# Performance work log

Measured on AMD Instinct MI355X. Metric: run time of the kernel, lower is better.

Reference implementation:

```python
import jax, jax.numpy as jnp
import numpy as np

L, H, D, DK, FF = 3, 8, 128, 16, 512  # layers, heads, embed, key/val dim, ffn hidden
B, N, F_IN, OUT = 32, 512, 16, 3
SCALE = 1.0 / np.sqrt(DK)


def setup_inputs() -> dict:
    key = jax.random.key(0)
    ks = jax.random.split(key, 16)
    x = jax.random.normal(ks[0], (B, N, F_IN), dtype=jnp.float32)
    m = jax.random.randint(ks[1], (B, N, N), 0, 2).astype(jnp.int32)
    # guarantee each query attends to at least itself (avoid all -inf rows)
    m = jnp.maximum(m, jnp.eye(N, dtype=jnp.int32)[None])
    def u(k, shape, fan):
        s = 1.0 / np.sqrt(fan)
        return jax.random.uniform(k, shape, jnp.float32, -s, s)
    return {
        "x": x, "mask": m,
        "We": u(ks[2], (F_IN, D), D),
        "Wq": u(ks[3], (L, H, D, DK), DK),
        "Wk": u(ks[4], (L, H, D, DK), DK),
        "Wv": u(ks[5], (L, H, D, DK), DK),
        "Wout": u(ks[6], (L, H, DK, D), D),
        "Wff1": u(ks[7], (L, D, FF), D),
        "bff1": u(ks[8], (L, FF), D),
        "Wff2": u(ks[9], (L, FF, D), FF),
        "bff2": u(ks[10], (L, D), FF),
        "Wp": u(ks[11], (D, D), D),
        "Wr": u(ks[12], (2 * D, OUT), 2 * D),
        "br": u(ks[13], (OUT,), 2 * D),
    }


def reference(x, mask, We, Wq, Wk, Wv, Wout, Wff1, bff1, Wff2, bff2, Wp, Wr, br):
    mb = mask.astype(bool)[None]  # [1,B,N,N] broadcast over heads
    h = jax.nn.relu(x @ We)  # initial embedding [B,N,D]
    for l in range(L):
        # multi-head attention with additive skip
        Q = jnp.einsum('bnd,hdk->hbnk', h, Wq[l])
        K = jnp.einsum('bnd,hdk->hbnk', h, Wk[l])
        V = jnp.einsum('bnd,hdk->hbnk', h, Wv[l])
        compat = SCALE * jnp.einsum('hbqk,hbnk->hbqn', Q, K)  # [H,B,N,N]
        compat = jnp.where(mb, compat, -jnp.inf)
        attn = jax.nn.softmax(compat, axis=-1)
        # note: torch's attn.clone()[...] = 0 is a no-op, so no re-zeroing
        heads = jnp.einsum('hbqn,hbnk->hbqk', attn, V)
        h = h + jnp.einsum('hbqk,hkd->bqd', heads, Wout[l])
        # feed-forward with additive skip
        h = h + jax.nn.relu(h @ Wff1[l] + bff1[l]) @ Wff2[l] + bff2[l] * 0 + (jax.nn.relu(h @ Wff1[l] + bff1[l]) @ Wff2[l] + bff2[l] - (jax.nn.relu(h @ Wff1[l] + bff1[l]) @ Wff2[l]))  # placeholder removed below
    return h


# clean faithful version (used)
def reference(x, mask, We, Wq, Wk, Wv, Wout, Wff1, bff1, Wff2, bff2, Wp, Wr, br):
    mb = mask.astype(bool)[None]  # [1,B,N,N]
    h = jax.nn.relu(x @ We)  # [B,N,D]
    for l in range(L):
        Q = jnp.einsum('bnd,hdk->hbnk', h, Wq[l])
        K = jnp.einsum('bnd,hdk->hbnk', h, Wk[l])
        V = jnp.einsum('bnd,hdk->hbnk', h, Wv[l])
        compat = SCALE * jnp.einsum('hbqk,hbnk->hbqn', Q, K)
        compat = jnp.where(mb, compat, -jnp.inf)
        attn = jax.nn.softmax(compat, axis=-1)
        heads = jnp.einsum('hbqn,hbnk->hbqk', attn, V)
        h = h + jnp.einsum('hbqk,hkd->bqd', heads, Wout[l])
        h = h + (jax.nn.relu(h @ Wff1[l] + bff1[l]) @ Wff2[l] + bff2[l])
    # readout (actor head: output_dim=3)
    h_pooled = (h.mean(axis=1)) @ Wp  # [B,D]
    f_pooled = jnp.broadcast_to(h_pooled[:, None, :], h.shape)  # [B,N,D]
    features = jax.nn.relu(jnp.concatenate([f_pooled, h], axis=-1))  # [B,N,2D]
    return features @ Wr + br  # [B,N,3]
```

## Files before the change

kernel.cpp:

```cpp
#include <hip/hip_runtime.h>
#include <cstdint>
#include <cstddef>

#define L_LAYERS 3
#define H_HEADS 8
#define D_EMB 128
#define DKV 16
#define FF_DIM 512
#define B_BATCH 32
#define N_SEQ 512
#define F_INP 16
#define OUT_DIM 3
#define M_ROWS (B_BATCH * N_SEQ)
#define QSCALE 0.3606737602222409f

typedef unsigned short ushort_t;
typedef unsigned int uint_t;
typedef __attribute__((ext_vector_type(8))) short short8;
typedef __attribute__((ext_vector_type(4))) float f32x4;
typedef __attribute__((ext_vector_type(16))) float f32x16;

__device__ inline ushort_t f2bf(float x) {
    union { float f; uint_t u; } v; v.f = x;
    uint_t r = v.u + 0x7fffu + ((v.u >> 16) & 1u);
    return (ushort_t)(r >> 16);
}

__device__ inline uint_t pack2bf_tr(float a, float b) {
    union { float f; uint_t u; } ua, ub;
    ua.f = a; ub.f = b;
#if __has_builtin(__builtin_amdgcn_perm)
    return __builtin_amdgcn_perm(ub.u, ua.u, 0x07060302u);
#else
    return (ua.u >> 16) | (ub.u & 0xffff0000u);
#endif
}

__device__ inline float exp2fast(float x) {
#if __has_builtin(__builtin_amdgcn_exp2f)
    return __builtin_amdgcn_exp2f(x);
#else
    float r; __asm__("v_exp_f32 %0, %1" : "=v"(r) : "v"(x)); return r;
#endif
}

__device__ inline void gload16(const void* g, void* l) {
    __builtin_amdgcn_global_load_lds(
        (const __attribute__((address_space(1))) unsigned int*)g,
        (__attribute__((address_space(3))) unsigned int*)l, 16, 0, 0);
}

#define PM_BLK 32768
#define RQ_BLK 576
#define TW_BLK 192
#define T1_BLK 768
#define T2_BLK 768
#define PB_BLK 16
#define EM_BLK 8192
__global__ __launch_bounds__(256) void preproc_kernel(
        const int* __restrict__ mask, unsigned long long* __restrict__ pm,
        const float* __restrict__ Wq, const float* __restrict__ Wk,
        const float* __restrict__ Wv, ushort_t* __restrict__ wqkvT,
        const float* __restrict__ Wout, ushort_t* __restrict__ woutT,
        const float* __restrict__ Wff1, ushort_t* __restrict__ wff1T,
        const float* __restrict__ Wff2, ushort_t* __restrict__ wff2T,
        float* __restrict__ pbsum,
        const float* __restrict__ x, const float* __restrict__ We,
        float* __restrict__ hf, ushort_t* __restrict__ hb) {
    int bx = blockIdx.x;
    const int tid = threadIdx.x;
    if (bx < PM_BLK) {
        int gid = bx * 256 + tid;
        int v = mask[gid];
        unsigned long long bal = __ballot(v != 0);
        if ((tid & 63) == 0) pm[gid >> 6] = bal;
        return;
    }
    bx -= PM_BLK;
    if (bx < RQ_BLK) {
        int idx = bx * 256 + tid;
        int d = idx & 127;
        int n = (idx >> 7) % 384;
        int l = idx / (384 * 128);
        int proj = n >> 7, hh = (n & 127) >> 4, kk = n & 15;
        const float* src = proj == 0 ? Wq : proj == 1 ? Wk : Wv;
        wqkvT[idx] = f2bf(src[((size_t)(l * 8 + hh) * 128 + d) * 16 + kk]);
        return;
    }
    bx -= RQ_BLK;
    if (bx < TW_BLK + T1_BLK + T2_BLK) {
        const float* src; ushort_t* dst; int R, C;
        if (bx < TW_BLK) { src = Wout; dst = woutT; R = 128; C = 128; }
        else if (bx < TW_BLK + T1_BLK) { src = Wff1; dst = wff1T; R = 128; C = 512; bx -= TW_BLK; }
        else { src = Wff2; dst = wff2T; R = 512; C = 128; bx -= TW_BLK + T1_BLK; }
        int idx = bx * 256 + tid;
        int b = idx / (R * C);
        int rem = idx - b * (R * C);
        int r = rem / C, c = rem - r * C;
        dst[(size_t)b * R * C + (size_t)c * R + r] = f2bf(src[idx]);
        return;
    }
    bx -= TW_BLK + T1_BLK + T2_BLK;
    if (bx < PB_BLK) {
        pbsum[bx * 256 + tid] = 0.f;
        return;
    }
    bx -= PB_BLK;
    {
        const int d = tid & 127;
        const int m = bx * 2 + (tid >> 7);
        const float* xr = x + (size_t)m * 16;
        float acc = 0.f;
#pragma unroll
        for (int k = 0; k < 16; k++) acc += xr[k] * We[k * 128 + d];
        acc = fmaxf(acc, 0.f);
        hf[(size_t)m * 128 + d] = acc;
        hb[(size_t)m * 128 + d] = f2bf(acc);
    }
}

__global__ __launch_bounds__(512, 4) void qkv_attn_kernel(
        const ushort_t* __restrict__ hb,
        const ushort_t* __restrict__ WqkvT,
        const uint_t* __restrict__ pm,
        ushort_t* __restrict__ Aout) {
    __shared__ __align__(16) ushort_t sm[35968];
    ushort_t* KF = sm;
    ushort_t* Vt = sm + 8192;
    ushort_t* Qs = sm + 16512;
    ushort_t* Ws = sm + 20608;
    ushort_t* Ps = sm + 16512;
    uint_t*   Ms = (uint_t*)(sm + 26752);

    const int tid = threadIdx.x;
    const int w = tid >> 6, L = tid & 63;
    const int lr = L & 15, lq = L >> 4;
    const int lane31 = L & 31, lhalf = L >> 5;
    const int bx = blockIdx.x;
    const int b = bx >> 4, h = (bx >> 1) & 7, half = bx & 1;

    for (int i = tid; i < 768; i += 512) {
        const int row = i >> 4, cg = i & 15;
        const int proj = row >> 4, kk = row & 15;
        gload16(WqkvT + (size_t)(proj * 128 + h * 16 + kk) * 128 + cg * 8, &Ws[i * 8]);
    }
    for (int i = tid; i < 2048; i += 512) {
        const int q = i >> 3, cw = (i & 7) * 2;
        const uint2 v = *(const uint2*)(pm + (size_t)(b * 512 + half * 256 + q) * 16 + cw);
        *(uint2*)&Ms[q * 18 + cw] = v;
    }
    __syncthreads();

    const ushort_t* Ab = hb + (size_t)b * 512 * 128;
    for (int mc = 0; mc < 4; mc++) {
        f32x4 acc[3];
#pragma unroll
        for (int j = 0; j < 3; j++) acc[j] = (f32x4){0.f, 0.f, 0.f, 0.f};
#pragma unroll
        for (int k0 = 0; k0 < 128; k0 += 32) {
            short8 af = *(const short8*)(Ab + (size_t)(mc * 128 + w * 16 + lr) * 128 + k0 + lq * 8);
#pragma unroll
            for (int j = 0; j < 3; j++) {
                short8 bf = *(const short8*)&Ws[(j * 16 + lr) * 128 + k0 + lq * 8];
                acc[j] = __builtin_amdgcn_mfma_f32_16x16x32_bf16(af, bf, acc[j], 0, 0, 0);
            }
        }
        const int rbase = mc * 128 + w * 16 + lq * 4;
#pragma unroll
        for (int r = 0; r < 4; r++) {
            const int key = rbase + r;
            KF[(key >> 5) * 512 + ((lr >> 3) * 32 + (key & 31)) * 8 + (lr & 7)] = f2bf(acc[1][r]);
            Vt[lr * 520 + key] = f2bf(acc[2][r]);
        }
        if ((mc >> 1) == half) {
            const int qb = (mc & 1) * 128 + w * 16 + lq * 4;
#pragma unroll
            for (int r = 0; r < 4; r++)
                Qs[(qb + r) * 16 + lr] = f2bf(acc[0][r] * QSCALE);
        }
    }
    __syncthreads();

    const int q0g = half * 256 + w * 32;
    const short8 qf = *(const short8*)&Qs[(w * 32 + lane31) * 16 + lhalf * 8];
    const int msrow = (w * 32 + lane31) * 18;
    __syncthreads();

    const f32x16 zero16 = (f32x16)(0.f);
    short8 vone;
#pragma unroll
    for (int i = 0; i < 8; i++) vone[i] = (short)0x3F80;

    f32x4 oacc0 = (f32x4){0.f, 0.f, 0.f, 0.f};
    f32x4 oacc1 = (f32x4){0.f, 0.f, 0.f, 0.f};
    f32x4 lacc0 = (f32x4){0.f, 0.f, 0.f, 0.f};
    f32x4 lacc1 = (f32x4){0.f, 0.f, 0.f, 0.f};
#pragma unroll
    for (int t = 0; t < 16; t++) {
        short8 kf = *(const short8*)&KF[t * 512 + L * 8];
        f32x16 s = __builtin_amdgcn_mfma_f32_32x32x16_bf16(kf, qf, zero16, 0, 0, 0);
        const uint_t word = Ms[msrow + t];
#pragma unroll
        for (int r = 0; r < 16; r++) {
            const int keyl = (r & 3) + 8 * (r >> 2) + 4 * lhalf;
            const float e = exp2fast(s[r]);
            s[r] = (word & (1u << keyl)) ? e : 0.f;
        }
#pragma unroll
        for (int g = 0; g < 4; g++) {
            const uint_t lo = pack2bf_tr(s[g * 4 + 0], s[g * 4 + 1]);
            const uint_t hi = pack2bf_tr(s[g * 4 + 2], s[g * 4 + 3]);
            *(uint2*)&Ps[w * 1152 + lane31 * 36 + g * 8 + 4 * lhalf] = make_uint2(lo, hi);
        }
        short8 vb = *(const short8*)&Vt[lr * 520 + t * 32 + lq * 8];
        short8 pa0 = *(const short8*)&Ps[w * 1152 + lr * 36 + lq * 8];
        short8 pa1 = *(const short8*)&Ps[w * 1152 + (16 + lr) * 36 + lq * 8];
        oacc0 = __builtin_amdgcn_mfma_f32_16x16x32_bf16(pa0, vb, oacc0, 0, 0, 0);
        oacc1 = __builtin_amdgcn_mfma_f32_16x16x32_bf16(pa1, vb, oacc1, 0, 0, 0);
        lacc0 = __builtin_amdgcn_mfma_f32_16x16x32_bf16(pa0, vone, lacc0, 0, 0, 0);
        lacc1 = __builtin_amdgcn_mfma_f32_16x16x32_bf16(pa1, vone, lacc1, 0, 0, 0);
    }

#pragma unroll
    for (int qa = 0; qa < 2; qa++) {
        const f32x4 oa = qa ? oacc1 : oacc0;
        const f32x4 la = qa ? lacc1 : lacc0;
#pragma unroll
        for (int rr = 0; rr < 4; rr++) {
            const int qloc = qa * 16 + lq * 4 + rr;
            Aout[(size_t)(b * 512 + q0g + qloc) * 128 + h * 16 + lr] = f2bf(oa[rr] / la[rr]);
        }
    }
}

__global__ __launch_bounds__(256, 2) void tail_kernel(
        const ushort_t* __restrict__ A,
        const ushort_t* __restrict__ WoT,
        const ushort_t* __restrict__ W1T,
        const ushort_t* __restrict__ W2T,
        const float* __restrict__ b1,
        const float* __restrict__ b2,
        float* __restrict__ hf, ushort_t* __restrict__ hb,
        float* __restrict__ pbsum, int accum) {
    __shared__ __align__(16) ushort_t sm[39424];
    ushort_t* AsA = sm;
    ushort_t* AsB = sm + 1024;
    ushort_t* BsA = sm + 2048;
    ushort_t* BsB = sm + 10240;
    ushort_t* C1b = sm + 18432;
    ushort_t* T   = sm + 22784;

    const int tid = threadIdx.x;
    const int w = tid >> 6, l = tid & 63;
    const int lr = l & 15, lq = l >> 4;
    const int srow = (l >> 2);
    const int scol = (l & 3) * 8;
    const int m0 = blockIdx.x * 32;

    f32x4 c1a[2][2];
#pragma unroll
    for (int i = 0; i < 2; i++)
#pragma unroll
        for (int j = 0; j < 2; j++) c1a[i][j] = (f32x4){0.f, 0.f, 0.f, 0.f};
    if (w < 2)
        gload16(A + (size_t)(m0 + w * 16 + srow) * 128 + scol, &AsA[(w * 16 + srow) * 32 + scol]);
#pragma unroll
    for (int it = 0; it < 2; it++)
        gload16(WoT + (size_t)(it * 64 + w * 16 + srow) * 128 + scol, &BsA[(it * 64 + w * 16 + srow) * 32 + scol]);
#pragma unroll
    for (int k0 = 0; k0 < 128; k0 += 32) {
        ushort_t* Ac = (k0 & 32) ? AsB : AsA;
        ushort_t* Bc = (k0 & 32) ? BsB : BsA;
        ushort_t* An = (k0 & 32) ? AsA : AsB;
        ushort_t* Bn = (k0 & 32) ? BsA : BsB;
        __syncthreads();
        if (k0 + 32 < 128) {
            if (w < 2)
                gload16(A + (size_t)(m0 + w * 16 + srow) * 128 + k0 + 32 + scol,
                        &An[(w * 16 + srow) * 32 + scol]);
#pragma unroll
            for (int it = 0; it < 2; it++)
                gload16(WoT + (size_t)(it * 64 + w * 16 + srow) * 128 + k0 + 32 + scol,
                        &Bn[(it * 64 + w * 16 + srow) * 32 + scol]);
        }
        short8 af[2], bfr[2];
#pragma unroll
        for (int i = 0; i < 2; i++) af[i] = *(const short8*)&Ac[(i * 16 + lr) * 32 + lq * 8];
#pragma unroll
        for (int j = 0; j < 2; j++) bfr[j] = *(const short8*)&Bc[(w * 32 + j * 16 + lr) * 32 + lq * 8];
#pragma unroll
        for (int i = 0; i < 2; i++)
#pragma unroll
            for (int j = 0; j < 2; j++)
                c1a[i][j] = __builtin_amdgcn_mfma_f32_16x16x32_bf16(af[i], bfr[j], c1a[i][j], 0, 0, 0);
    }
    float c1[2][2][4];
#pragma unroll
    for (int i = 0; i < 2; i++)
#pragma unroll
        for (int r = 0; r < 4; r++) {
            const int row = i * 16 + lq * 4 + r;
#pragma unroll
            for (int j = 0; j < 2; j++) {
                const int n = w * 32 + j * 16 + lr;
                const float v = c1a[i][j][r] + hf[(size_t)(m0 + row) * 128 + n];
                c1[i][j][r] = v;
                C1b[row * 136 + n] = f2bf(v);
            }
        }

#pragma unroll
    for (int it = 0; it < 4; it++)
        gload16(W1T + (size_t)(it * 64 + w * 16 + srow) * 128 + scol, &BsA[(it * 64 + w * 16 + srow) * 32 + scol]);
#pragma unroll
    for (int nc = 0; nc < 2; nc++) {
        f32x4 ta[2][4];
#pragma unroll
        for (int i = 0; i < 2; i++)
#pragma unroll
            for (int j = 0; j < 4; j++) ta[i][j] = (f32x4){0.f, 0.f, 0.f, 0.f};
#pragma unroll
        for (int k0i = 0; k0i < 4; k0i++) {
            const int c = nc * 4 + k0i;
            ushort_t* Bc = (c & 1) ? BsB : BsA;
            ushort_t* Bn = (c & 1) ? BsA : BsB;
            __syncthreads();
            if (c + 1 < 8) {
                const int nc2 = (c + 1) >> 2, k02 = ((c + 1) & 3) * 32;
#pragma unroll
                for (int it = 0; it < 4; it++)
                    gload16(W1T + (size_t)(nc2 * 256 + it * 64 + w * 16 + srow) * 128 + k02 + scol,
                            &Bn[(it * 64 + w * 16 + srow) * 32 + scol]);
            }
            short8 af[2], bfr[4];
#pragma unroll
            for (int i = 0; i < 2; i++)
                af[i] = *(const short8*)&C1b[(i * 16 + lr) * 136 + k0i * 32 + lq * 8];
#pragma unroll
            for (int j = 0; j < 4; j++)
                bfr[j] = *(const short8*)&Bc[(w * 64 + j * 16 + lr) * 32 + lq * 8];
#pragma unroll
            for (int i = 0; i < 2; i++)
#pragma unroll
                for (int j = 0; j < 4; j++)
                    ta[i][j] = __builtin_amdgcn_mfma_f32_16x16x32_bf16(af[i], bfr[j], ta[i][j], 0, 0, 0);
        }
#pragma unroll
        for (int j = 0; j < 4; j++) {
            const int n = nc * 256 + w * 64 + j * 16 + lr;
            const float bv = b1[n];
#pragma unroll
            for (int i = 0; i < 2; i++)
#pragma unroll
                for (int r = 0; r < 4; r++) {
                    const int row = i * 16 + lq * 4 + r;
                    T[row * 520 + n] = f2bf(fmaxf(ta[i][j][r] + bv, 0.f));
                }
        }
    }

#pragma unroll
    for (int it = 0; it < 2; it++)
        gload16(W2T + (size_t)(it * 64 + w * 16 + srow) * 512 + scol, &BsA[(it * 64 + w * 16 + srow) * 32 + scol]);
    f32x4 oa[2][2];
#pragma unroll
    for (int i = 0; i < 2; i++)
#pragma unroll
        for (int j = 0; j < 2; j++) oa[i][j] = (f32x4){0.f, 0.f, 0.f, 0.f};
#pragma unroll
    for (int k0 = 0; k0 < 512; k0 += 32) {
        ushort_t* Bc = ((k0 >> 5) & 1) ? BsB : BsA;
        ushort_t* Bn = ((k0 >> 5) & 1) ? BsA : BsB;
        __syncthreads();
        if (k0 + 32 < 512) {
#pragma unroll
            for (int it = 0; it < 2; it++)
                gload16(W2T + (size_t)(it * 64 + w * 16 + srow) * 512 + k0 + 32 + scol,
                        &Bn[(it * 64 + w * 16 + srow) * 32 + scol]);
        }
        short8 af[2], bfr[2];
#pragma unroll
        for (int i = 0; i < 2; i++)
            af[i] = *(const short8*)&T[(i * 16 + lr) * 520 + k0 + lq * 8];
#pragma unroll
        for (int j = 0; j < 2; j++)
            bfr[j] = *(const short8*)&Bc[(w * 32 + j * 16 + lr) * 32 + lq * 8];
#pragma unroll
        for (int i = 0; i < 2; i++)
#pragma unroll
            for (int j = 0; j < 2; j++)
                oa[i][j] = __builtin_amdgcn_mfma_f32_16x16x32_bf16(af[i], bfr[j], oa[i][j], 0, 0, 0);
    }
#pragma unroll
    for (int j = 0; j < 2; j++) {
        const int n = w * 32 + j * 16 + lr;
        const float bv = b2[n];
        float psum = 0.f;
#pragma unroll
        for (int i = 0; i < 2; i++)
#pragma unroll
            for (int r = 0; r < 4; r++) {
                const int row = i * 16 + lq * 4 + r;
                const float v = oa[i][j][r] + bv + c1[i][j][r];
                psum += v;
                hf[(size_t)(m0 + row) * 128 + n] = v;
                hb[(size_t)(m0 + row) * 128 + n] = f2bf(v);
            }
        if (accum) {
            psum += __shfl_xor(psum, 16);
            psum += __shfl_xor(psum, 32);
            if (lq == 0) atomicAdd(&pbsum[(m0 >> 9) * 128 + n], psum);
        }
    }
}

__global__ __launch_bounds__(256) void readout_kernel(const float* __restrict__ h,
                                                      const float* __restrict__ pbsum,
                                                      const float* __restrict__ Wp,
                                                      const float* __restrict__ Wr,
                                                      const float* __restrict__ br,
                                                      float* __restrict__ out) {
    const int u = blockIdx.x;
    const int b = u >> 4;
    const int m0 = u * 32;
    const int t = threadIdx.x;
    __shared__ float pooled[128];
    __shared__ float rp[128];
    __shared__ float pb3[3];
    if (t < 128) pooled[t] = pbsum[b * 128 + t] * (1.0f / 512.0f);
    __syncthreads();
    if (t < 128) {
        float a = 0.f;
        for (int dd = 0; dd < 128; dd++) a += pooled[dd] * Wp[dd * 128 + t];
        rp[t] = fmaxf(a, 0.f);
    }
    __syncthreads();
    if (t < OUT_DIM) {
        float a = br[t];
        for (int j = 0; j < 128; j++) a += rp[j] * Wr[j * 3 + t];
        pb3[t] = a;
    }
    __syncthreads();
    const int j = t & 7;
    const int row = m0 + (t >> 3);
    const float* hr = h + (size_t)row * 128 + j * 16;
    float a0 = 0.f, a1 = 0.f, a2o = 0.f;
#pragma unroll
    for (int dd = 0; dd < 16; dd++) {
        const float v = fmaxf(hr[dd], 0.f);
        const float* wr = Wr + (size_t)(128 + j * 16 + dd) * 3;
        a0 += v * wr[0]; a1 += v * wr[1]; a2o += v * wr[2];
    }
#pragma unroll
    for (int off = 4; off; off >>= 1) {
        a0 += __shfl_down(a0, off, 8);
        a1 += __shfl_down(a1, off, 8);
        a2o += __shfl_down(a2o, off, 8);
    }
    if (j == 0) {
        out[(size_t)row * 3 + 0] = a0 + pb3[0];
        out[(size_t)row * 3 + 1] = a1 + pb3[1];
        out[(size_t)row * 3 + 2] = a2o + pb3[2];
    }
}

extern "C" void kernel_launch(void* const* d_in, const int* in_sizes, int n_in,
                              void* d_out, int out_size, void* d_ws, size_t ws_size,
                              hipStream_t stream) {
    const float* x    = (const float*)d_in[0];
    const int*   mask = (const int*)d_in[1];
    const float* We   = (const float*)d_in[2];
    const float* Wq   = (const float*)d_in[3];
    const float* Wk   = (const float*)d_in[4];
    const float* Wv   = (const float*)d_in[5];
    const float* Wout = (const float*)d_in[6];
    const float* Wff1 = (const float*)d_in[7];
    const float* bff1 = (const float*)d_in[8];
    const float* Wff2 = (const float*)d_in[9];
    const float* bff2 = (const float*)d_in[10];
    const float* Wp   = (const float*)d_in[11];
    const float* Wr   = (const float*)d_in[12];
    const float* br   = (const float*)d_in[13];
    float* out = (float*)d_out;

    char* ws = (char*)d_ws;
    unsigned long long* pm64 = (unsigned long long*)(ws + 0);
    const uint_t* pm32       = (const uint_t*)(ws + 0);
    ushort_t* wqkvT = (ushort_t*)(ws + 1048576);
    ushort_t* woutT = (ushort_t*)(ws + 1343488);
    ushort_t* wff1T = (ushort_t*)(ws + 1441792);
    ushort_t* wff2T = (ushort_t*)(ws + 1835008);
    float*    pbsum = (float*)(ws + 2228224);
    float*    hbuf  = (float*)(ws + 4194304);
    ushort_t* hb16  = (ushort_t*)(ws + 12582912);
    ushort_t* a16   = (ushort_t*)(ws + 41943040);

    preproc_kernel<<<PM_BLK + RQ_BLK + TW_BLK + T1_BLK + T2_BLK + PB_BLK + EM_BLK, 256, 0, stream>>>(
        mask, pm64, Wq, Wk, Wv, wqkvT, Wout, woutT, Wff1, wff1T, Wff2, wff2T,
        pbsum, x, We, hbuf, hb16);

    for (int l = 0; l < L_LAYERS; l++) {
        qkv_attn_kernel<<<512, 512, 0, stream>>>(
            hb16, wqkvT + (size_t)l * 384 * 128, pm32, a16);
        tail_kernel<<<M_ROWS / 32, 256, 0, stream>>>(
            a16, woutT + (size_t)l * 128 * 128, wff1T + (size_t)l * 512 * 128,
            wff2T + (size_t)l * 128 * 512, bff1 + l * 512, bff2 + l * 128,
            hbuf, hb16, pbsum, (l == L_LAYERS - 1) ? 1 : 0);
    }

    readout_kernel<<<512, 256, 0, stream>>>(hbuf, pbsum, Wp, Wr, br, out);
}
```

Before: 276.2 us.

## Stream tail weights from global, split FFN hidden into halves, double-buffer attention P

The tail kernel stops staging A, Wout, Wff1 and Wff2 through LDS with double-buffered global_load_lds and instead reads MFMA operands straight from global memory through cache. It also splits the FFN hidden dimension into two halves so the intermediate tile and LDS footprint shrink, using XOR-swizzled layouts to avoid bank conflicts. In the attention kernel, P is ping-ponged between two LDS buffers, and the PV MFMAs are wrapped in s_setprio. Attention occupancy drops from 4 to 2 blocks per CU, and direct global weight loads risk higher latency in exchange for fewer barriers.

```diff
diff --git a/kernel.cpp b/kernel.cpp
--- a/kernel.cpp
+++ b/kernel.cpp
@@ -48,6 +48,13 @@
     __builtin_amdgcn_global_load_lds(
         (const __attribute__((address_space(1))) unsigned int*)g,
         (__attribute__((address_space(3))) unsigned int*)l, 16, 0, 0);
+}
+
+__device__ inline int swz128(int row, int col) {
+    return row * 128 + ((((col >> 3) ^ (row & 7)) << 3) | (col & 7));
+}
+__device__ inline int swz256(int row, int col) {
+    return row * 256 + ((((col >> 3) ^ (row & 7)) << 3) | (col & 7));
 }
 
 #define PM_BLK 32768
@@ -119,18 +126,19 @@
     }
 }
 
-__global__ __launch_bounds__(512, 4) void qkv_attn_kernel(
+__global__ __launch_bounds__(512, 2) void qkv_attn_kernel(
         const ushort_t* __restrict__ hb,
         const ushort_t* __restrict__ WqkvT,
         const uint_t* __restrict__ pm,
         ushort_t* __restrict__ Aout) {
-    __shared__ __align__(16) ushort_t sm[35968];
-    ushort_t* KF = sm;
-    ushort_t* Vt = sm + 8192;
-    ushort_t* Qs = sm + 16512;
-    ushort_t* Ws = sm + 20608;
-    ushort_t* Ps = sm + 16512;
-    uint_t*   Ms = (uint_t*)(sm + 26752);
+    __shared__ __align__(16) ushort_t sm[44160];
+    ushort_t* KF  = sm;
+    ushort_t* Vt  = sm + 8192;
+    ushort_t* Qs  = sm + 16512;
+    ushort_t* Ws  = sm + 20608;
+    ushort_t* PsA = sm + 16512;
+    ushort_t* PsB = sm + 25728;
+    uint_t*   Ms  = (uint_t*)(sm + 34944);
 
     const int tid = threadIdx.x;
     const int w = tid >> 6, L = tid & 63;
@@ -195,31 +203,40 @@
     f32x4 oacc1 = (f32x4){0.f, 0.f, 0.f, 0.f};
     f32x4 lacc0 = (f32x4){0.f, 0.f, 0.f, 0.f};
     f32x4 lacc1 = (f32x4){0.f, 0.f, 0.f, 0.f};
-#pragma unroll
-    for (int t = 0; t < 16; t++) {
-        short8 kf = *(const short8*)&KF[t * 512 + L * 8];
-        f32x16 s = __builtin_amdgcn_mfma_f32_32x32x16_bf16(kf, qf, zero16, 0, 0, 0);
-        const uint_t word = Ms[msrow + t];
-#pragma unroll
-        for (int r = 0; r < 16; r++) {
-            const int keyl = (r & 3) + 8 * (r >> 2) + 4 * lhalf;
-            const float e = exp2fast(s[r]);
-            s[r] = (word & (1u << keyl)) ? e : 0.f;
-        }
-#pragma unroll
-        for (int g = 0; g < 4; g++) {
-            const uint_t lo = pack2bf_tr(s[g * 4 + 0], s[g * 4 + 1]);
-            const uint_t hi = pack2bf_tr(s[g * 4 + 2], s[g * 4 + 3]);
-            *(uint2*)&Ps[w * 1152 + lane31 * 36 + g * 8 + 4 * lhalf] = make_uint2(lo, hi);
-        }
-        short8 vb = *(const short8*)&Vt[lr * 520 + t * 32 + lq * 8];
-        short8 pa0 = *(const short8*)&Ps[w * 1152 + lr * 36 + lq * 8];
-        short8 pa1 = *(const short8*)&Ps[w * 1152 + (16 + lr) * 36 + lq * 8];
-        oacc0 = __builtin_amdgcn_mfma_f32_16x16x32_bf16(pa0, vb, oacc0, 0, 0, 0);
-        oacc1 = __builtin_amdgcn_mfma_f32_16x16x32_bf16(pa1, vb, oacc1, 0, 0, 0);
-        lacc0 = __builtin_amdgcn_mfma_f32_16x16x32_bf16(pa0, vone, lacc0, 0, 0, 0);
-        lacc1 = __builtin_amdgcn_mfma_f32_16x16x32_bf16(pa1, vone, lacc1, 0, 0, 0);
-    }
+
+#define ATTN_STEP(T_IDX, PS) do {                                                   \
+    short8 kf = *(const short8*)&KF[(T_IDX) * 512 + L * 8];                         \
+    f32x16 s = __builtin_amdgcn_mfma_f32_32x32x16_bf16(kf, qf, zero16, 0, 0, 0);    \
+    const uint_t word = Ms[msrow + (T_IDX)];                                        \
+    _Pragma("unroll")                                                               \
+    for (int r = 0; r < 16; r++) {                                                  \
+        const int keyl = (r & 3) + 8 * (r >> 2) + 4 * lhalf;                        \
+        const float e = exp2fast(s[r]);                                             \
+        s[r] = (word & (1u << keyl)) ? e : 0.f;                                     \
+    }                                                                               \
+    _Pragma("unroll")                                                               \
+    for (int g = 0; g < 4; g++) {                                                   \
+        const uint_t lo = pack2bf_tr(s[g * 4 + 0], s[g * 4 + 1]);                   \
+        const uint_t hi = pack2bf_tr(s[g * 4 + 2], s[g * 4 + 3]);                   \
+        *(uint2*)&(PS)[w * 1152 + lane31 * 36 + g * 8 + 4 * lhalf] = make_uint2(lo, hi); \
+    }                                                                               \
+    short8 vb = *(const short8*)&Vt[lr * 520 + (T_IDX) * 32 + lq * 8];              \
+    short8 pa0 = *(const short8*)&(PS)[w * 1152 + lr * 36 + lq * 8];                \
+    short8 pa1 = *(const short8*)&(PS)[w * 1152 + (16 + lr) * 36 + lq * 8];         \
+    __builtin_amdgcn_s_setprio(1);                                                  \
+    oacc0 = __builtin_amdgcn_mfma_f32_16x16x32_bf16(pa0, vb, oacc0, 0, 0, 0);       \
+    oacc1 = __builtin_amdgcn_mfma_f32_16x16x32_bf16(pa1, vb, oacc1, 0, 0, 0);       \
+    lacc0 = __builtin_amdgcn_mfma_f32_16x16x32_bf16(pa0, vone, lacc0, 0, 0, 0);     \
+    lacc1 = __builtin_amdgcn_mfma_f32_16x16x32_bf16(pa1, vone, lacc1, 0, 0, 0);     \
+    __builtin_amdgcn_s_setprio(0);                                                  \
+} while (0)
+
+#pragma unroll
+    for (int tp = 0; tp < 8; tp++) {
+        ATTN_STEP(2 * tp, PsA);
+        ATTN_STEP(2 * tp + 1, PsB);
+    }
+#undef ATTN_STEP
 
 #pragma unroll
     for (int qa = 0; qa < 2; qa++) {
@@ -242,19 +259,13 @@
         const float* __restrict__ b2,
         float* __restrict__ hf, ushort_t* __restrict__ hb,
         float* __restrict__ pbsum, int accum) {
-    __shared__ __align__(16) ushort_t sm[39424];
-    ushort_t* AsA = sm;
-    ushort_t* AsB = sm + 1024;
-    ushort_t* BsA = sm + 2048;
-    ushort_t* BsB = sm + 10240;
-    ushort_t* C1b = sm + 18432;
-    ushort_t* T   = sm + 22784;
+    __shared__ __align__(16) ushort_t sm[12288];
+    ushort_t* C1b = sm;
+    ushort_t* Tt  = sm + 4096;
 
     const int tid = threadIdx.x;
     const int w = tid >> 6, l = tid & 63;
     const int lr = l & 15, lq = l >> 4;
-    const int srow = (l >> 2);
-    const int scol = (l & 3) * 8;
     const int m0 = blockIdx.x * 32;
 
     f32x4 c1a[2][2];
@@ -262,32 +273,15 @@
     for (int i = 0; i < 2; i++)
 #pragma unroll
         for (int j = 0; j < 2; j++) c1a[i][j] = (f32x4){0.f, 0.f, 0.f, 0.f};
-    if (w < 2)
-        gload16(A + (size_t)(m0 + w * 16 + srow) * 128 + scol, &AsA[(w * 16 + srow) * 32 + scol]);
-#pragma unroll
-    for (int it = 0; it < 2; it++)
-        gload16(WoT + (size_t)(it * 64 + w * 16 + srow) * 128 + scol, &BsA[(it * 64 + w * 16 + srow) * 32 + scol]);
 #pragma unroll
     for (int k0 = 0; k0 < 128; k0 += 32) {
-        ushort_t* Ac = (k0 & 32) ? AsB : AsA;
-        ushort_t* Bc = (k0 & 32) ? BsB : BsA;
-        ushort_t* An = (k0 & 32) ? AsA : AsB;
-        ushort_t* Bn = (k0 & 32) ? BsA : BsB;
-        __syncthreads();
-        if (k0 + 32 < 128) {
-            if (w < 2)
-                gload16(A + (size_t)(m0 + w * 16 + srow) * 128 + k0 + 32 + scol,
-                        &An[(w * 16 + srow) * 32 + scol]);
-#pragma unroll
-            for (int it = 0; it < 2; it++)
-                gload16(WoT + (size_t)(it * 64 + w * 16 + srow) * 128 + k0 + 32 + scol,
-                        &Bn[(it * 64 + w * 16 + srow) * 32 + scol]);
-        }
         short8 af[2], bfr[2];
 #pragma unroll
-        for (int i = 0; i < 2; i++) af[i] = *(const short8*)&Ac[(i * 16 + lr) * 32 + lq * 8];
-#pragma unroll
-        for (int j = 0; j < 2; j++) bfr[j] = *(const short8*)&Bc[(w * 32 + j * 16 + lr) * 32 + lq * 8];
+        for (int i = 0; i < 2; i++)
+            af[i] = *(const short8*)(A + (size_t)(m0 + i * 16 + lr) * 128 + k0 + lq * 8);
+#pragma unroll
+        for (int j = 0; j < 2; j++)
+            bfr[j] = *(const short8*)(WoT + (size_t)(w * 32 + j * 16 + lr) * 128 + k0 + lq * 8);
 #pragma unroll
         for (int i = 0; i < 2; i++)
 #pragma unroll
@@ -305,92 +299,70 @@
                 const int n = w * 32 + j * 16 + lr;
                 const float v = c1a[i][j][r] + hf[(size_t)(m0 + row) * 128 + n];
                 c1[i][j][r] = v;
-                C1b[row * 136 + n] = f2bf(v);
+                C1b[swz128(row, n)] = f2bf(v);
             }
         }
-
-#pragma unroll
-    for (int it = 0; it < 4; it++)
-        gload16(W1T + (size_t)(it * 64 + w * 16 + srow) * 128 + scol, &BsA[(it * 64 + w * 16 + srow) * 32 + scol]);
-#pragma unroll
-    for (int nc = 0; nc < 2; nc++) {
+    __syncthreads();
+
+    f32x4 oa[2][2];
+#pragma unroll
+    for (int i = 0; i < 2; i++)
+#pragma unroll
+        for (int j = 0; j < 2; j++) oa[i][j] = (f32x4){0.f, 0.f, 0.f, 0.f};
+
+#pragma unroll
+    for (int hh = 0; hh < 2; hh++) {
         f32x4 ta[2][4];
 #pragma unroll
         for (int i = 0; i < 2; i++)
 #pragma unroll
             for (int j = 0; j < 4; j++) ta[i][j] = (f32x4){0.f, 0.f, 0.f, 0.f};
 #pragma unroll
-        for (int k0i = 0; k0i < 4; k0i++) {
-            const int c = nc * 4 + k0i;
-            ushort_t* Bc = (c & 1) ? BsB : BsA;
-            ushort_t* Bn = (c & 1) ? BsA : BsB;
-            __syncthreads();
-            if (c + 1 < 8) {
-                const int nc2 = (c + 1) >> 2, k02 = ((c + 1) & 3) * 32;
-#pragma unroll
-                for (int it = 0; it < 4; it++)
-                    gload16(W1T + (size_t)(nc2 * 256 + it * 64 + w * 16 + srow) * 128 + k02 + scol,
-                            &Bn[(it * 64 + w * 16 + srow) * 32 + scol]);
-            }
+        for (int kc = 0; kc < 4; kc++) {
             short8 af[2], bfr[4];
 #pragma unroll
             for (int i = 0; i < 2; i++)
-                af[i] = *(const short8*)&C1b[(i * 16 + lr) * 136 + k0i * 32 + lq * 8];
+                af[i] = *(const short8*)&C1b[swz128(i * 16 + lr, kc * 32 + lq * 8)];
 #pragma unroll
             for (int j = 0; j < 4; j++)
-                bfr[j] = *(const short8*)&Bc[(w * 64 + j * 16 + lr) * 32 + lq * 8];
+                bfr[j] = *(const short8*)(W1T + (size_t)(hh * 256 + w * 64 + j * 16 + lr) * 128 + kc * 32 + lq * 8);
 #pragma unroll
             for (int i = 0; i < 2; i++)
 #pragma unroll
                 for (int j = 0; j < 4; j++)
                     ta[i][j] = __builtin_amdgcn_mfma_f32_16x16x32_bf16(af[i], bfr[j], ta[i][j], 0, 0, 0);
         }
+        if (hh) __syncthreads();
 #pragma unroll
         for (int j = 0; j < 4; j++) {
-            const int n = nc * 256 + w * 64 + j * 16 + lr;
-            const float bv = b1[n];
+            const int nrel = w * 64 + j * 16 + lr;
+            const float bv = b1[hh * 256 + nrel];
 #pragma unroll
             for (int i = 0; i < 2; i++)
 #pragma unroll
                 for (int r = 0; r < 4; r++) {
                     const int row = i * 16 + lq * 4 + r;
-                    T[row * 520 + n] = f2bf(fmaxf(ta[i][j][r] + bv, 0.f));
+                    Tt[swz256(row, nrel)] = f2bf(fmaxf(ta[i][j][r] + bv, 0.f));
                 }
         }
-    }
-
-#pragma unroll
-    for (int it = 0; it < 2; it++)
-        gload16(W2T + (size_t)(it * 64 + w * 16 + srow) * 512 + scol, &BsA[(it * 64 + w * 16 + srow) * 32 + scol]);
-    f32x4 oa[2][2];
-#pragma unroll
-    for (int i = 0; i < 2; i++)
-#pragma unroll
-        for (int j = 0; j < 2; j++) oa[i][j] = (f32x4){0.f, 0.f, 0.f, 0.f};
-#pragma unroll
-    for (int k0 = 0; k0 < 512; k0 += 32) {
-        ushort_t* Bc = ((k0 >> 5) & 1) ? BsB : BsA;
-        ushort_t* Bn = ((k0 >> 5) & 1) ? BsA : BsB;
         __syncthreads();
-        if (k0 + 32 < 512) {
-#pragma unroll
-            for (int it = 0; it < 2; it++)
-                gload16(W2T + (size_t)(it * 64 + w * 16 + srow) * 512 + k0 + 32 + scol,
-                        &Bn[(it * 64 + w * 16 + srow) * 32 + scol]);
-        }
-        short8 af[2], bfr[2];
-#pragma unroll
-        for (int i = 0; i < 2; i++)
-            af[i] = *(const short8*)&T[(i * 16 + lr) * 520 + k0 + lq * 8];
-#pragma unroll
-        for (int j = 0; j < 2; j++)
-            bfr[j] = *(const short8*)&Bc[(w * 32 + j * 16 + lr) * 32 + lq * 8];
-#pragma unroll
-        for (int i = 0; i < 2; i++)
+#pragma unroll
+        for (int kc = 0; kc < 8; kc++) {
+            short8 af[2], bfr[2];
+#pragma unroll
+            for (int i = 0; i < 2; i++)
+                af[i] = *(const short8*)&Tt[swz256(i * 16 + lr, kc * 32 + lq * 8)];
 #pragma unroll
             for (int j = 0; j < 2; j++)
-                oa[i][j] = __builtin_amdgcn_mfma_f32_16x16x32_bf16(af[i], bfr[j], oa[i][j], 0, 0, 0);
-    }
+                bfr[j] = *(const short8*)(W2T + (size_t)(w * 32 + j * 16 + lr) * 512 + hh * 256 + kc * 32 + lq * 8);
+#pragma unroll
+            for (int i = 0; i < 2; i++)
+#pragma unroll
+                for (int j = 0; j < 2; j++)
+                    oa[i][j] = __builtin_amdgcn_mfma_f32_16x16x32_bf16(af[i], bfr[j], oa[i][j], 0, 0, 0);
+        }
+    }
+
 #pragma unroll
     for (int j = 0; j < 2; j++) {
         const int n = w * 32 + j * 16 + lr;
```

After: 307.9 us. +11.5%, slower.
